# Kernel optimization log

Hardware: AMD Instinct MI355X
Metric: run time of the kernel (lower is better)

## Reference

```python
import jax, jax.numpy as jnp
import numpy as np

N, D, E, OUT = 10000, 15, 320, 30
H_INOUT = 5  # n_heads for in/out attention layers


def mha(q, k, v, wqkv, bqkv, wo, bo, nheads):
    # q,k,v: [B, L, E]; torch.nn.MultiheadAttention math (unbatched per node)
    B, L, Ed = q.shape
    hd = Ed // nheads
    wq, wk, wv = jnp.split(wqkv, 3, axis=0)
    bq, bk, bv = jnp.split(bqkv, 3)
    q2 = (q @ wq.T + bq).reshape(B, L, nheads, hd)
    k2 = (k @ wk.T + bk).reshape(B, -1, nheads, hd)
    v2 = (v @ wv.T + bv).reshape(B, -1, nheads, hd)
    scores = jnp.einsum('blhd,bmhd->bhlm', q2, k2) * (hd ** -0.5)
    a = jax.nn.softmax(scores, axis=-1)
    o = jnp.einsum('bhlm,bmhd->blhd', a, v2).reshape(B, L, Ed)
    return o @ wo.T + bo


def attn_layer(seq, Wq, Wk, Wv, wqkv, bqkv, wo, bo, nheads):
    # AttentionLayer: custom Q/K/V projections then MultiheadAttention
    return mha(seq @ Wq, seq @ Wk, seq @ Wv, wqkv, bqkv, wo, bo, nheads)


def setup_inputs() -> dict:
    key = jax.random.key(0)
    ks = jax.random.split(key, 24)
    s = 0.05  # scale params small for numerically stable softmax
    inp = {
        'X': jax.random.normal(ks[0], (N, E), jnp.float32),
        'in_idx': jax.random.randint(ks[1], (N, D), 0, N),
        'out_idx': jax.random.randint(ks[2], (N, D), 0, N),
        'in_Wq': jax.random.uniform(ks[3], (E, E)) * s,
        'in_Wk': jax.random.uniform(ks[4], (E, E)) * s,
        'in_Wv': jax.random.uniform(ks[5], (E, E)) * s,
        'in_qkv_w': jax.random.normal(ks[6], (3 * E, E)) * s,
        'in_qkv_b': jax.random.normal(ks[7], (3 * E,)) * s,
        'in_o_w': jax.random.normal(ks[8], (E, E)) * s,
        'in_o_b': jax.random.normal(ks[9], (E,)) * s,
        'out_Wq': jax.random.uniform(ks[10], (E, E)) * s,
        'out_Wk': jax.random.uniform(ks[11], (E, E)) * s,
        'out_Wv': jax.random.uniform(ks[12], (E, E)) * s,
        'out_qkv_w': jax.random.normal(ks[13], (3 * E, E)) * s,
        'out_qkv_b': jax.random.normal(ks[14], (3 * E,)) * s,
        'out_o_w': jax.random.normal(ks[15], (E, E)) * s,
        'out_o_b': jax.random.normal(ks[16], (E,)) * s,
        'fin_qkv_w': jax.random.normal(ks[17], (3 * E, E)) * s,
        'fin_qkv_b': jax.random.normal(ks[18], (3 * E,)) * s,
        'fin_o_w': jax.random.normal(ks[19], (E, E)) * s,
        'fin_o_b': jax.random.normal(ks[20], (E,)) * s,
        'W': jax.random.uniform(ks[21], (E, OUT)) * s,
    }
    return inp


def reference(X, in_idx, out_idx, in_Wq, in_Wk, in_Wv, in_qkv_w, in_qkv_b,
              in_o_w, in_o_b, out_Wq, out_Wk, out_Wv, out_qkv_w, out_qkv_b,
              out_o_w, out_o_b, fin_qkv_w, fin_qkv_b, fin_o_w, fin_o_b, W):
    # per-node sequence: [self ; neighbors] -> [N, D+1, E]
    seq_in = jnp.concatenate([X[:, None, :], X[in_idx]], axis=1)
    seq_out = jnp.concatenate([X[:, None, :], X[out_idx]], axis=1)
    a_in = attn_layer(seq_in, in_Wq, in_Wk, in_Wv, in_qkv_w, in_qkv_b,
                      in_o_w, in_o_b, H_INOUT)
    a_out = attn_layer(seq_out, out_Wq, out_Wk, out_Wv, out_qkv_w, out_qkv_b,
                       out_o_w, out_o_b, H_INOUT)
    att = jnp.concatenate([a_in, a_out], axis=1)  # [N, 2(D+1), E]
    fin = mha(att, att, att, fin_qkv_w, fin_qkv_b, fin_o_w, fin_o_b, 1)
    # first token of final attention per node -> project -> ELU
    return jax.nn.elu(fin[:, 0, :] @ W)
```

## Files before the change

kernel.cpp:

```cpp
#include <hip/hip_runtime.h>
#include <hip/hip_bf16.h>

typedef __hip_bfloat16 bf16;
typedef __bf16 nbf;
typedef nbf bf16x8 __attribute__((ext_vector_type(8)));
typedef float f32x4 __attribute__((ext_vector_type(4)));

#define NNODE 10000
#define DDEG  15
#define EE    320
#define LL    16
#define NH    5
#define HD    64
#define OUTD  30
#define PCOLS 1920
#define KF    642

__global__ void detect_dtype_kernel(const unsigned int* __restrict__ X, int* __restrict__ flag)
{
    __shared__ int cnt;
    if (threadIdx.x == 0) cnt = 0;
    __syncthreads();
    int local = 0;
    for (int i = threadIdx.x; i < 1024; i += 256) {
        unsigned int lo = X[i] & 0xFFFFu;
        int e = (int)((lo >> 7) & 0xFFu);
        if (e >= 100 && e <= 140) local++;
    }
    atomicAdd(&cnt, local);
    __syncthreads();
    if (threadIdx.x == 0) *flag = (cnt > 512) ? 1 : 0;
}

__global__ void convert_bf_kernel(const void* __restrict__ src, nbf* __restrict__ dst,
                                  int n, const int* __restrict__ flag)
{
    int i = blockIdx.x * 256 + threadIdx.x;
    if (i >= n) return;
    if (*flag) dst[i] = ((const nbf*)src)[i];
    else       dst[i] = (nbf)(((const float*)src)[i]);
}

#define NSEG 18
struct ConvTab {
    const void* src[NSEG];
    void*       dst[NSEG];
    int         n[NSEG];
    int         tobf[NSEG];
};

__global__ void convert_batch_kernel(ConvTab t, const int* __restrict__ flag)
{
    const int seg = blockIdx.y;
    const int i = blockIdx.x * 256 + threadIdx.x;
    if (i >= t.n[seg]) return;
    float v = (*flag) ? (float)(((const nbf*)t.src[seg])[i]) : ((const float*)t.src[seg])[i];
    if (t.tobf[seg]) ((nbf*)t.dst[seg])[i] = (nbf)v;
    else             ((float*)t.dst[seg])[i] = v;
}

__global__ __launch_bounds__(256) void transpose3_kernel(const void* s0, const void* s1,
        const void* s2, nbf* __restrict__ dstbase, const int* __restrict__ flag)
{
    const void* src = (blockIdx.z == 0) ? s0 : (blockIdx.z == 1) ? s1 : s2;
    nbf* dst = dstbase + (size_t)blockIdx.z * EE * EE;
    __shared__ nbf tile[32][33];
    const int bx = blockIdx.x * 32, by = blockIdx.y * 32;
    const int tx = threadIdx.x & 31, ty = threadIdx.x >> 5;
    const int f = *flag;
    #pragma unroll
    for (int i = 0; i < 4; ++i) {
        const int r = by + ty + i * 8;
        float v = f ? (float)(((const nbf*)src)[(long)r * EE + bx + tx])
                    : ((const float*)src)[(long)r * EE + bx + tx];
        tile[ty + i * 8][tx] = (nbf)v;
    }
    __syncthreads();
    #pragma unroll
    for (int i = 0; i < 4; ++i) {
        const int r = bx + ty + i * 8;
        dst[(long)r * EE + by + tx] = tile[tx][ty + i * 8];
    }
}

__device__ __forceinline__ void stor(float* p, float v) { *p = v; }
__device__ __forceinline__ void stor(bf16* p, float v) { *p = __float2bfloat16(v); }

template<bool AT, bool BT, typename OT>
__global__ __launch_bounds__(256) void gemm_k(const float* __restrict__ A, int lda,
                       const float* __restrict__ B, int ldb,
                       const float* __restrict__ bias,
                       OT* __restrict__ C, int ldc, int M, int Nn, int K)
{
    __shared__ float As[16][65];
    __shared__ float Bs[16][65];
    const int tid = threadIdx.x;
    const int tx = tid & 15, ty = tid >> 4;
    const int n0 = blockIdx.x * 64, m0 = blockIdx.y * 64;
    float acc[4][4] = {};
    for (int k0 = 0; k0 < K; k0 += 16) {
        if constexpr (AT) {
            for (int i = tid; i < 1024; i += 256) {
                int kk = i >> 6, r = i & 63;
                int gm = m0 + r, gk = k0 + kk;
                As[kk][r] = (gm < M && gk < K) ? A[(long)gk * lda + gm] : 0.f;
            }
        } else {
            for (int i = tid; i < 1024; i += 256) {
                int r = i >> 4, kk = i & 15;
                int gm = m0 + r, gk = k0 + kk;
                As[kk][r] = (gm < M && gk < K) ? A[(long)gm * lda + gk] : 0.f;
            }
        }
        if constexpr (BT) {
            for (int i = tid; i < 1024; i += 256) {
                int r = i >> 4, kk = i & 15;
                int gn = n0 + r, gk = k0 + kk;
                Bs[kk][r] = (gn < Nn && gk < K) ? B[(long)gn * ldb + gk] : 0.f;
            }
        } else {
            for (int i = tid; i < 1024; i += 256) {
                int kk = i >> 6, c = i & 63;
                int gk = k0 + kk, gn = n0 + c;
                Bs[kk][c] = (gk < K && gn < Nn) ? B[(long)gk * ldb + gn] : 0.f;
            }
        }
        __syncthreads();
        #pragma unroll
        for (int kk = 0; kk < 16; ++kk) {
            float ra[4], rb[4];
            #pragma unroll
            for (int a = 0; a < 4; ++a) ra[a] = As[kk][ty * 4 + a];
            #pragma unroll
            for (int b = 0; b < 4; ++b) rb[b] = Bs[kk][tx * 4 + b];
            #pragma unroll
            for (int a = 0; a < 4; ++a)
                #pragma unroll
                for (int b = 0; b < 4; ++b)
                    acc[a][b] += ra[a] * rb[b];
        }
        __syncthreads();
    }
    #pragma unroll
    for (int a = 0; a < 4; ++a) {
        int gm = m0 + ty * 4 + a;
        if (gm >= M) continue;
        #pragma unroll
        for (int b = 0; b < 4; ++b) {
            int gn = n0 + tx * 4 + b;
            if (gn >= Nn) continue;
            float v = acc[a][b] + (bias ? bias[gn] : 0.f);
            stor(&C[(long)gm * ldc + gn], v);
        }
    }
}

template<typename OT>
__global__ __launch_bounds__(256) void gemm_mfma(const nbf* __restrict__ A, int lda,
        const nbf* __restrict__ Bt, int ldb, const float* __restrict__ bias,
        OT* __restrict__ C, int ldc, int M, int Nn, int K)
{
    __shared__ __align__(16) nbf As[128][40];
    __shared__ __align__(16) nbf Bs[128][40];
    const int tid = threadIdx.x;
    const int lane = tid & 63, wave = tid >> 6;
    const int wr = (wave >> 1) * 64, wc = (wave & 1) * 64;
    const int m0 = blockIdx.y * 128, n0 = blockIdx.x * 128;
    const int lr = lane & 15, lq = lane >> 4;
    f32x4 acc[4][4];
    #pragma unroll
    for (int i = 0; i < 4; ++i)
        #pragma unroll
        for (int j = 0; j < 4; ++j) { acc[i][j][0]=0.f; acc[i][j][1]=0.f; acc[i][j][2]=0.f; acc[i][j][3]=0.f; }

    for (int k0 = 0; k0 < K; k0 += 32) {
        #pragma unroll
        for (int v = tid; v < 512; v += 256) {
            const int row = v >> 2, cv = (v & 3) << 3;
            const int gk = k0 + cv;
            {
                const int gm = m0 + row;
                bf16x8 val;
                if (gm < M && gk + 8 <= K) {
                    val = *(const bf16x8*)(A + (long)gm * lda + gk);
                } else {
                    union { bf16x8 v8; nbf e[8]; } u;
                    #pragma unroll
                    for (int j = 0; j < 8; ++j) {
                        float x = (gm < M && gk + j < K) ? (float)A[(long)gm * lda + gk + j] : 0.f;
                        u.e[j] = (nbf)x;
                    }
                    val = u.v8;
                }
                *(bf16x8*)&As[row][cv] = val;
            }
            {
                const int gn = n0 + row;
                bf16x8 val;
                if (gn < Nn && gk + 8 <= K) {
                    val = *(const bf16x8*)(Bt + (long)gn * ldb + gk);
                } else {
                    union { bf16x8 v8; nbf e[8]; } u;
                    #pragma unroll
                    for (int j = 0; j < 8; ++j) {
                        float x = (gn < Nn && gk + j < K) ? (float)Bt[(long)gn * ldb + gk + j] : 0.f;
                        u.e[j] = (nbf)x;
                    }
                    val = u.v8;
                }
                *(bf16x8*)&Bs[row][cv] = val;
            }
        }
        __syncthreads();
        bf16x8 af[4], bfv[4];
        #pragma unroll
        for (int i = 0; i < 4; ++i) af[i] = *(const bf16x8*)&As[wr + i * 16 + lr][lq * 8];
        #pragma unroll
        for (int j = 0; j < 4; ++j) bfv[j] = *(const bf16x8*)&Bs[wc + j * 16 + lr][lq * 8];
        #pragma unroll
        for (int i = 0; i < 4; ++i)
            #pragma unroll
            for (int j = 0; j < 4; ++j)
                acc[i][j] = __builtin_amdgcn_mfma_f32_16x16x32_bf16(af[i], bfv[j], acc[i][j], 0, 0, 0);
        __syncthreads();
    }
    #pragma unroll
    for (int i = 0; i < 4; ++i) {
        #pragma unroll
        for (int j = 0; j < 4; ++j) {
            const int gn = n0 + wc + j * 16 + lr;
            if (gn >= Nn) continue;
            const float bv = bias ? bias[gn] : 0.f;
            #pragma unroll
            for (int r = 0; r < 4; ++r) {
                const int gm = m0 + wr + i * 16 + lq * 4 + r;
                if (gm < M) stor(&C[(long)gm * ldc + gn], acc[i][j][r] + bv);
            }
        }
    }
}

#define NJOB 11
struct JobTab {
    const nbf* A[NJOB];
    const nbf* B[NJOB];
    nbf*       C[NJOB];
};

__global__ __launch_bounds__(256) void gemm_mfma_jobs(JobTab jt)
{
    const nbf* A  = jt.A[blockIdx.z];
    const nbf* Bt = jt.B[blockIdx.z];
    nbf* C        = jt.C[blockIdx.z];
    __shared__ __align__(16) nbf As[128][40];
    __shared__ __align__(16) nbf Bs[128][40];
    const int tid = threadIdx.x;
    const int lane = tid & 63, wave = tid >> 6;
    const int wr = (wave >> 1) * 64, wc = (wave & 1) * 64;
    const int m0 = blockIdx.y * 128, n0 = blockIdx.x * 128;
    const int lr = lane & 15, lq = lane >> 4;
    f32x4 acc[4][4];
    #pragma unroll
    for (int i = 0; i < 4; ++i)
        #pragma unroll
        for (int j = 0; j < 4; ++j) { acc[i][j][0]=0.f; acc[i][j][1]=0.f; acc[i][j][2]=0.f; acc[i][j][3]=0.f; }
    for (int k0 = 0; k0 < EE; k0 += 32) {
        #pragma unroll
        for (int v = tid; v < 512; v += 256) {
            const int row = v >> 2, cv = (v & 3) << 3;
            const int gk = k0 + cv;
            const int gm = m0 + row, gn = n0 + row;
            bf16x8 va = {}, vb = {};
            if (gm < EE) va = *(const bf16x8*)(A + (long)gm * EE + gk);
            if (gn < EE) vb = *(const bf16x8*)(Bt + (long)gn * EE + gk);
            *(bf16x8*)&As[row][cv] = va;
            *(bf16x8*)&Bs[row][cv] = vb;
        }
        __syncthreads();
        bf16x8 af[4], bfv[4];
        #pragma unroll
        for (int i = 0; i < 4; ++i) af[i] = *(const bf16x8*)&As[wr + i * 16 + lr][lq * 8];
        #pragma unroll
        for (int j = 0; j < 4; ++j) bfv[j] = *(const bf16x8*)&Bs[wc + j * 16 + lr][lq * 8];
        #pragma unroll
        for (int i = 0; i < 4; ++i)
            #pragma unroll
            for (int j = 0; j < 4; ++j)
                acc[i][j] = __builtin_amdgcn_mfma_f32_16x16x32_bf16(af[i], bfv[j], acc[i][j], 0, 0, 0);
        __syncthreads();
    }
    #pragma unroll
    for (int i = 0; i < 4; ++i)
        #pragma unroll
        for (int j = 0; j < 4; ++j) {
            const int gn = n0 + wc + j * 16 + lr;
            if (gn >= EE) continue;
            #pragma unroll
            for (int r = 0; r < 4; ++r) {
                const int gm = m0 + wr + i * 16 + lq * 4 + r;
                if (gm < EE) C[(long)gm * EE + gn] = (nbf)acc[i][j][r];
            }
        }
}

__global__ __launch_bounds__(320) void compose_bias_kernel(
        const float* __restrict__ in_o_b, const float* __restrict__ out_o_b,
        const float* __restrict__ fin_qkv_w, const float* __restrict__ fin_qkv_b,
        float* __restrict__ bqc_in, nbf* __restrict__ Kcat, nbf* __restrict__ VcatN)
{
    const int which = blockIdx.x;
    const int b = threadIdx.x;
    const float* ob = (which == 2 || which == 4) ? out_o_b : in_o_b;
    const int off = (which == 0) ? 0 : (which <= 2) ? 320 : 640;
    float acc = fin_qkv_b[off + b];
    const float* wr = fin_qkv_w + (long)(off + b) * EE;
    for (int e = 0; e < EE; ++e) acc += ob[e] * wr[e];
    if (which == 0)      bqc_in[b] = acc;
    else if (which == 1) Kcat[(long)640 * EE + b] = (nbf)acc;
    else if (which == 2) Kcat[(long)641 * EE + b] = (nbf)acc;
    else if (which == 3) VcatN[(long)640 * EE + b] = (nbf)acc;
    else                 VcatN[(long)641 * EE + b] = (nbf)acc;
}

__global__ void compose_bfin(const float* __restrict__ fin_o_b, const float* __restrict__ W,
                             float* __restrict__ bfin)
{
    int j = threadIdx.x;
    if (j >= OUTD) return;
    float acc = 0.f;
    for (int e = 0; e < EE; ++e) acc += fin_o_b[e] * W[e * OUTD + j];
    bfin[j] = acc;
}

__global__ void compose_bT(const float* __restrict__ bqc, const nbf* __restrict__ Kcat,
                           float* __restrict__ bT)
{
    int c = blockIdx.x * 256 + threadIdx.x;
    if (c >= KF) return;
    const nbf* kr = Kcat + (long)c * EE;
    float acc = 0.f;
    for (int b = 0; b < EE; ++b) acc += bqc[b] * (float)kr[b];
    bT[c] = acc;
}

__global__ void ut_prep_kernel(const float* __restrict__ WWT, nbf* __restrict__ Ut)
{
    int v = blockIdx.x * 256 + threadIdx.x;
    if (v >= 64 * EE) return;
    int n = v / EE, e = v % EE;
    float val = 0.f;
    if (n < OUTD) val = WWT[(long)n * KF + e];
    else if (n >= 32 && n < 32 + OUTD) val = WWT[(long)(n - 32) * KF + 320 + e];
    Ut[v] = (nbf)val;
}

__global__ __launch_bounds__(320) void attn1_kernel(const nbf* __restrict__ P,
                const int* __restrict__ in_idx, const int* __restrict__ out_idx,
                nbf* __restrict__ O, int node_base)
{
    const int bx = blockIdx.x;
    const int lnode = bx >> 1, dir = bx & 1;
    const int node = node_base + lnode;
    const int tid = threadIdx.x;
    const int lane = tid & 63, wave = tid >> 6;
    __shared__ __align__(16) nbf v_s[16][328];
    __shared__ __align__(16) nbf p_s[NH][16][16];
    const int* idx = dir ? out_idx : in_idx;
    const long coloff = (long)dir * 960;
    const int lr = lane & 15, lq = lane >> 4;
    #pragma unroll
    for (int v = tid; v < 640; v += 320) {
        const int row = v / 40, c8 = (v % 40) * 8;
        const int src = (row == 0) ? node : idx[node * DDEG + row - 1];
        *(bf16x8*)&v_s[row][c8] = *(const bf16x8*)(P + (long)src * PCOLS + coloff + 640 + c8);
    }
    const int msrc = (lr == 0) ? node : idx[node * DDEG + lr - 1];
    const nbf* prow = P + (long)msrc * PCOLS + coloff;
    f32x4 sc = {0.f, 0.f, 0.f, 0.f};
    #pragma unroll
    for (int c = 0; c < 2; ++c) {
        bf16x8 aq = *(const bf16x8*)(prow + wave * 64 + c * 32 + lq * 8);
        bf16x8 bk = *(const bf16x8*)(prow + 320 + wave * 64 + c * 32 + lq * 8);
        sc = __builtin_amdgcn_mfma_f32_16x16x32_bf16(aq, bk, sc, 0, 0, 0);
    }
    float pr[4], mx[4], sm[4];
    #pragma unroll
    for (int r = 0; r < 4; ++r) { pr[r] = sc[r] * 0.125f; mx[r] = pr[r]; }
    #pragma unroll
    for (int msk = 8; msk >= 1; msk >>= 1)
        #pragma unroll
        for (int r = 0; r < 4; ++r) mx[r] = fmaxf(mx[r], __shfl_xor(mx[r], msk));
    #pragma unroll
    for (int r = 0; r < 4; ++r) { pr[r] = __expf(pr[r] - mx[r]); sm[r] = pr[r]; }
    #pragma unroll
    for (int msk = 8; msk >= 1; msk >>= 1)
        #pragma unroll
        for (int r = 0; r < 4; ++r) sm[r] += __shfl_xor(sm[r], msk);
    #pragma unroll
    for (int r = 0; r < 4; ++r) p_s[wave][lq * 4 + r][lr] = (nbf)(pr[r] / sm[r]);
    union { bf16x8 v8; nbf e[8]; } pf;
    #pragma unroll
    for (int j = 0; j < 8; ++j) pf.e[j] = (nbf)0.f;
    if (lq < 2) pf.v8 = *(const bf16x8*)&p_s[wave][lr][lq * 8];
    __syncthreads();
    nbf* orow = O + (long)lnode * (32 * EE) + dir * (16 * EE);
    #pragma unroll
    for (int t = 0; t < 4; ++t) {
        const int e0 = wave * 64 + t * 16;
        union { bf16x8 v8; nbf e[8]; } af;
        #pragma unroll
        for (int j = 0; j < 8; ++j) af.e[j] = (nbf)0.f;
        if (lq < 2) {
            #pragma unroll
            for (int j = 0; j < 8; ++j) af.e[j] = v_s[lq * 8 + j][e0 + lr];
        }
        f32x4 ov = {0.f, 0.f, 0.f, 0.f};
        ov = __builtin_amdgcn_mfma_f32_16x16x32_bf16(af.v8, pf.v8, ov, 0, 0, 0);
        union { unsigned long long u; nbf e[4]; } o4;
        #pragma unroll
        for (int r = 0; r < 4; ++r) o4.e[r] = (nbf)ov[r];
        *(unsigned long long*)(orow + lr * EE + e0 + lq * 4) = o4.u;
    }
}

__global__ __launch_bounds__(256) void final_mega_kernel(const nbf* __restrict__ O,
        const float* __restrict__ T, const nbf* __restrict__ Ut,
        const float* __restrict__ WWT, const float* __restrict__ bfin,
        void* __restrict__ out, long obase, int ncnt, const int* __restrict__ flag)
{
    const int i0 = blockIdx.x * 4;
    const int tid = threadIdx.x;
    const int lane = tid & 63, wave = tid >> 6;
    const int node = i0 + wave;
    const int nodec = (node < ncnt) ? node : (ncnt - 1);
    __shared__ float t_s[4][KF];
    __shared__ float s_lds[4][32];
    for (int v = tid; v < 4 * KF; v += 256) {
        const int nn = v / KF;
        const int nc = (i0 + nn < ncnt) ? (i0 + nn) : (ncnt - 1);
        t_s[nn][v % KF] = T[(long)nc * KF + (v % KF)];
    }
    __syncthreads();
    const int lr = lane & 15, lq = lane >> 4;
    const nbf* obase_p = O + (long)nodec * (32 * EE);
    f32x4 acc[2][2];
    #pragma unroll
    for (int a = 0; a < 2; ++a)
        #pragma unroll
        for (int b = 0; b < 2; ++b) { acc[a][b][0]=0.f; acc[a][b][1]=0.f; acc[a][b][2]=0.f; acc[a][b][3]=0.f; }
    float s_part[2] = {0.f, 0.f};
    #pragma unroll
    for (int k0 = 0; k0 < EE; k0 += 32) {
        bf16x8 af[2], bfv[4];
        #pragma unroll
        for (int mt = 0; mt < 2; ++mt)
            af[mt] = *(const bf16x8*)(obase_p + (long)(mt * 16 + lr) * EE + k0 + lq * 8);
        #pragma unroll
        for (int nt = 0; nt < 4; ++nt)
            bfv[nt] = *(const bf16x8*)(Ut + (long)(nt * 16 + lr) * EE + k0 + lq * 8);
        #pragma unroll
        for (int mt = 0; mt < 2; ++mt)
            #pragma unroll
            for (int pp = 0; pp < 2; ++pp)
                acc[mt][pp] = __builtin_amdgcn_mfma_f32_16x16x32_bf16(af[mt], bfv[mt * 2 + pp], acc[mt][pp], 0, 0, 0);
        #pragma unroll
        for (int mt = 0; mt < 2; ++mt) {
            const float* tp = &t_s[wave][mt * 320 + k0 + lq * 8];
            #pragma unroll
            for (int j = 0; j < 8; ++j) s_part[mt] += (float)af[mt][j] * tp[j];
        }
    }
    #pragma unroll
    for (int mt = 0; mt < 2; ++mt) {
        s_part[mt] += __shfl_xor(s_part[mt], 16);
        s_part[mt] += __shfl_xor(s_part[mt], 32);
    }
    if (lq == 0) {
        s_lds[wave][lr]      = (s_part[0] + t_s[wave][640]) * 0.05590169943749474f;
        s_lds[wave][16 + lr] = (s_part[1] + t_s[wave][641]) * 0.05590169943749474f;
    }
    __syncthreads();
    float mx = -1e30f;
    #pragma unroll 4
    for (int m = 0; m < 32; ++m) mx = fmaxf(mx, s_lds[wave][m]);
    float esum = 0.f, a_in = 0.f, a_out = 0.f;
    #pragma unroll 4
    for (int m = 0; m < 32; ++m) {
        float e = __expf(s_lds[wave][m] - mx);
        esum += e;
        if (m < 16) a_in += e; else a_out += e;
    }
    const float inv = 1.f / esum;
    a_in *= inv; a_out *= inv;
    float pj[2] = {0.f, 0.f};
    #pragma unroll
    for (int r = 0; r < 4; ++r) {
        float A0 = __expf(s_lds[wave][lq * 4 + r] - mx) * inv;
        float A1 = __expf(s_lds[wave][16 + lq * 4 + r] - mx) * inv;
        pj[0] += A0 * acc[0][0][r] + A1 * acc[1][0][r];
        pj[1] += A0 * acc[0][1][r] + A1 * acc[1][1][r];
    }
    #pragma unroll
    for (int pp = 0; pp < 2; ++pp) {
        pj[pp] += __shfl_xor(pj[pp], 16);
        pj[pp] += __shfl_xor(pj[pp], 32);
    }
    if (lq == 0 && node < ncnt) {
        #pragma unroll
        for (int h = 0; h < 2; ++h) {
            const int j = h * 16 + lr;
            if (j < OUTD) {
                float r = pj[h] + a_in * WWT[(long)j * KF + 640]
                        + a_out * WWT[(long)j * KF + 641] + bfin[j];
                r = r > 0.f ? r : expm1f(r);
                if (*flag) ((bf16*)out)[obase + (long)node * OUTD + j] = __float2bfloat16(r);
                else       ((float*)out)[obase + (long)node * OUTD + j] = r;
            }
        }
    }
}

extern "C" void kernel_launch(void* const* d_in, const int* in_sizes, int n_in,
                              void* d_out, int out_size, void* d_ws, size_t ws_size,
                              hipStream_t stream)
{
    const int* in_idx  = (const int*)d_in[1];
    const int* out_idx = (const int*)d_in[2];

    char* p = (char*)d_ws;
    auto alloc = [&](size_t bytes) { char* r = p; p += (bytes + 255) & ~(size_t)255; return r; };
    const size_t EE2 = (size_t)EE * EE;
    int*   flag       = (int*)alloc(256);
    nbf*   X_bf       = (nbf*)alloc((size_t)NNODE * EE * 2);
    nbf*   qkvw6_bf   = (nbf*)alloc(6 * EE2 * 2);
    nbf*   Wg6_bf     = (nbf*)alloc(6 * EE2 * 2);
    nbf*   qkvw_fin_bf= (nbf*)alloc(3 * EE2 * 2);
    nbf*   owT        = (nbf*)alloc(3 * EE2 * 2);
    float* qkvw_fin_f = (float*)alloc(3 * EE2 * 4);
    float* qkvb_fin_f = (float*)alloc(3 * EE * 4);
    float* bcat       = (float*)alloc(PCOLS * 4);
    float* ob_in_f    = (float*)alloc(EE * 4);
    float* ob_out_f   = (float*)alloc(EE * 4);
    float* ob_fin_f   = (float*)alloc(EE * 4);
    float* W_f        = (float*)alloc((size_t)EE * OUTD * 4);
    float* ow_fin_f   = (float*)alloc(EE2 * 4);
    nbf*   AcatT  = (nbf*)alloc((size_t)PCOLS * EE * 2);
    nbf*   Qc_bf  = (nbf*)alloc(EE2 * 2);
    nbf*   Kcat   = (nbf*)alloc((size_t)KF * EE * 2);
    float* bqc_in = (float*)alloc(EE * 4);
    nbf*   M2T    = (nbf*)alloc((size_t)KF * EE * 2);
    float* bT     = (float*)alloc(KF * 4);
    nbf*   VcatN  = (nbf*)alloc((size_t)KF * EE * 2);
    nbf*   WfinT  = (nbf*)alloc((size_t)OUTD * EE * 2);
    float* WWT    = (float*)alloc((size_t)OUTD * KF * 4);
    float* bfin   = (float*)alloc(64 * 4);
    nbf*   Ut     = (nbf*)alloc((size_t)64 * EE * 2);
    nbf*   P      = (nbf*)alloc((size_t)NNODE * PCOLS * 2);
    size_t fixed = (size_t)(p - (char*)d_ws);

    const size_t per_node = (size_t)32 * EE * 2 + (size_t)KF * 4;
    size_t avail = (ws_size > fixed + 65536) ? (ws_size - fixed - 65536) : 0;
    long chunk_l = (long)(avail / (per_node + 8));
    chunk_l = (chunk_l / 4) * 4;
    int chunk = (chunk_l > NNODE) ? NNODE : (chunk_l < 4 ? 4 : (int)chunk_l);
    nbf*   O_c    = (nbf*)alloc((size_t)chunk * 32 * EE * 2);
    float* T_c    = (float*)alloc((size_t)chunk * KF * 4);

    dim3 blk(256);
    detect_dtype_kernel<<<1, blk, 0, stream>>>((const unsigned int*)d_in[0], flag);
    convert_bf_kernel<<<(NNODE * EE + 255) / 256, blk, 0, stream>>>(d_in[0], X_bf, NNODE * EE, flag);
    ConvTab ct;
    int s = 0;
    auto seg = [&](const void* src, void* dst, int n, int tobf) {
        ct.src[s] = src; ct.dst[s] = dst; ct.n[s] = n; ct.tobf[s] = tobf; ++s;
    };
    seg(d_in[6],  qkvw6_bf,           (int)(3 * EE2), 1);
    seg(d_in[13], qkvw6_bf + 3 * EE2, (int)(3 * EE2), 1);
    seg(d_in[3],  Wg6_bf + 0 * EE2, (int)EE2, 1);
    seg(d_in[4],  Wg6_bf + 1 * EE2, (int)EE2, 1);
    seg(d_in[5],  Wg6_bf + 2 * EE2, (int)EE2, 1);
    seg(d_in[10], Wg6_bf + 3 * EE2, (int)EE2, 1);
    seg(d_in[11], Wg6_bf + 4 * EE2, (int)EE2, 1);
    seg(d_in[12], Wg6_bf + 5 * EE2, (int)EE2, 1);
    seg(d_in[17], qkvw_fin_bf, (int)(3 * EE2), 1);
    seg(d_in[17], qkvw_fin_f,  (int)(3 * EE2), 0);
    seg(d_in[18], qkvb_fin_f, 3 * EE, 0);
    seg(d_in[7],  bcat,       3 * EE, 0);
    seg(d_in[14], bcat + 960, 3 * EE, 0);
    seg(d_in[9],  ob_in_f,  EE, 0);
    seg(d_in[16], ob_out_f, EE, 0);
    seg(d_in[20], ob_fin_f, EE, 0);
    seg(d_in[21], W_f, EE * OUTD, 0);
    seg(d_in[19], ow_fin_f, (int)EE2, 0);
    convert_batch_kernel<<<dim3((3 * (int)EE2 + 255) / 256, NSEG), blk, 0, stream>>>(ct, flag);
    transpose3_kernel<<<dim3(10, 10, 3), blk, 0, stream>>>(d_in[8], d_in[15], d_in[19], owT, flag);

    JobTab jt;
    for (int g = 0; g < 6; ++g) {
        jt.A[g] = qkvw6_bf + (size_t)g * EE2;
        jt.B[g] = Wg6_bf + (size_t)g * EE2;
        jt.C[g] = AcatT + (size_t)g * EE2;
    }
    jt.A[6] = owT;             jt.B[6] = qkvw_fin_bf;                      jt.C[6] = Qc_bf;
    jt.A[7] = owT;             jt.B[7] = qkvw_fin_bf + (size_t)320 * EE;   jt.C[7] = Kcat;
    jt.A[8] = owT + EE2;       jt.B[8] = qkvw_fin_bf + (size_t)320 * EE;   jt.C[8] = Kcat + (size_t)320 * EE;
    jt.A[9] = owT;             jt.B[9] = qkvw_fin_bf + (size_t)640 * EE;   jt.C[9] = VcatN;
    jt.A[10]= owT + EE2;       jt.B[10]= qkvw_fin_bf + (size_t)640 * EE;   jt.C[10]= VcatN + (size_t)320 * EE;
    gemm_mfma_jobs<<<dim3(3, 3, NJOB), blk, 0, stream>>>(jt);
    compose_bias_kernel<<<5, 320, 0, stream>>>(ob_in_f, ob_out_f, qkvw_fin_f, qkvb_fin_f,
                                               bqc_in, Kcat, VcatN);
    gemm_mfma<bf16><<<dim3(3, 6), blk, 0, stream>>>(
        Kcat, EE, Qc_bf, EE, nullptr, (bf16*)M2T, EE, KF, EE, EE);
    compose_bT<<<3, blk, 0, stream>>>(bqc_in, Kcat, bT);
    gemm_k<true, false, bf16><<<dim3(5, 1), blk, 0, stream>>>(
        W_f, OUTD, ow_fin_f, EE, nullptr, (bf16*)WfinT, EE, OUTD, EE, EE);
    gemm_mfma<float><<<dim3(6, 1), blk, 0, stream>>>(
        WfinT, EE, VcatN, EE, nullptr, WWT, KF, OUTD, KF, EE);
    compose_bfin<<<1, 64, 0, stream>>>(ob_fin_f, W_f, bfin);
    ut_prep_kernel<<<(64 * EE + 255) / 256, blk, 0, stream>>>(WWT, Ut);

    gemm_mfma<bf16><<<dim3(PCOLS / 128, (NNODE + 127) / 128), blk, 0, stream>>>(
        X_bf, EE, AcatT, EE, bcat, (bf16*)P, PCOLS, NNODE, PCOLS, EE);

    for (int base = 0; base < NNODE; base += chunk) {
        int cnt = (NNODE - base < chunk) ? (NNODE - base) : chunk;
        attn1_kernel<<<2 * cnt, dim3(320), 0, stream>>>(P, in_idx, out_idx, O_c, base);
        gemm_mfma<float><<<dim3((KF + 127) / 128, (cnt + 127) / 128), blk, 0, stream>>>(
            O_c, 32 * EE, M2T, EE, bT, T_c, KF, cnt, KF, EE);
        final_mega_kernel<<<(cnt + 3) / 4, blk, 0, stream>>>(
            O_c, T_c, Ut, WWT, bfin, d_out, (long)base * OUTD, cnt, flag);
    }
}
```

Baseline: 587.7 us.

## Fuse first-stage attention with final attention and avoid materializing O

Adds a small row0 kernel that computes only the first query token of the in-attention, which is all the final query projection needs. The T GEMM then runs on one row per node instead of the full 32-row O tensor. A single mega kernel per node recomputes both first-stage attentions, keeps the 32x320 outputs in shared memory, and runs the final softmax and output projection in place. This removes the large O round-trip through global memory and the chunked launch loop, at the cost of duplicating some first-stage attention work and using more shared memory per block.

```diff
diff --git a/kernel.cpp b/kernel.cpp
--- a/kernel.cpp
+++ b/kernel.cpp
@@ -15,6 +15,7 @@
 #define OUTD  30
 #define PCOLS 1920
 #define KF    642
+#define TST   644
 
 __global__ void detect_dtype_kernel(const unsigned int* __restrict__ X, int* __restrict__ flag)
 {
@@ -354,168 +355,187 @@
     Ut[v] = (nbf)val;
 }
 
-__global__ __launch_bounds__(320) void attn1_kernel(const nbf* __restrict__ P,
-                const int* __restrict__ in_idx, const int* __restrict__ out_idx,
-                nbf* __restrict__ O, int node_base)
-{
-    const int bx = blockIdx.x;
-    const int lnode = bx >> 1, dir = bx & 1;
-    const int node = node_base + lnode;
+__global__ __launch_bounds__(256) void row0_kernel(const nbf* __restrict__ P,
+        const int* __restrict__ in_idx, nbf* __restrict__ Orow0)
+{
+    const int tid = threadIdx.x, lane = tid & 63, wave = tid >> 6;
+    const int node = blockIdx.x * 4 + wave;
+    __shared__ float a_sh[4][16];
+    __shared__ int srcs_sh[4][16];
+    const int m = lane & 15, q4 = lane >> 4;
+    const int src = (m == 0) ? node : in_idx[node * DDEG + m - 1];
+    if (q4 == 0) srcs_sh[wave][m] = src;
+    const nbf* qrow = P + (long)node * PCOLS;
+    const nbf* krow = P + (long)src * PCOLS + 320;
+    #pragma unroll
+    for (int h = 0; h < NH; ++h) {
+        float s = 0.f;
+        bf16x8 q1 = *(const bf16x8*)(qrow + h * 64 + q4 * 16);
+        bf16x8 q2 = *(const bf16x8*)(qrow + h * 64 + q4 * 16 + 8);
+        bf16x8 k1 = *(const bf16x8*)(krow + h * 64 + q4 * 16);
+        bf16x8 k2 = *(const bf16x8*)(krow + h * 64 + q4 * 16 + 8);
+        #pragma unroll
+        for (int j = 0; j < 8; ++j)
+            s += (float)q1[j] * (float)k1[j] + (float)q2[j] * (float)k2[j];
+        s += __shfl_xor(s, 16);
+        s += __shfl_xor(s, 32);
+        s *= 0.125f;
+        float mxv = s;
+        #pragma unroll
+        for (int msk = 8; msk >= 1; msk >>= 1) mxv = fmaxf(mxv, __shfl_xor(mxv, msk));
+        float e = __expf(s - mxv);
+        float es = e;
+        #pragma unroll
+        for (int msk = 8; msk >= 1; msk >>= 1) es += __shfl_xor(es, msk);
+        if (q4 == 0) a_sh[wave][m] = e / es;
+        float o = 0.f;
+        #pragma unroll
+        for (int mm = 0; mm < 16; ++mm)
+            o += a_sh[wave][mm] * (float)P[(long)srcs_sh[wave][mm] * PCOLS + 640 + h * 64 + lane];
+        Orow0[(long)node * EE + h * 64 + lane] = (nbf)o;
+    }
+}
+
+__global__ __launch_bounds__(320) void mega_attn_kernel(const nbf* __restrict__ P,
+        const int* __restrict__ in_idx, const int* __restrict__ out_idx,
+        const float* __restrict__ T, const nbf* __restrict__ Ut,
+        const float* __restrict__ WWT, const float* __restrict__ bfin,
+        void* __restrict__ out, const int* __restrict__ flag)
+{
+    const int node = blockIdx.x;
     const int tid = threadIdx.x;
     const int lane = tid & 63, wave = tid >> 6;
+    __shared__ __align__(16) nbf o_s[32][328];
     __shared__ __align__(16) nbf v_s[16][328];
     __shared__ __align__(16) nbf p_s[NH][16][16];
-    const int* idx = dir ? out_idx : in_idx;
-    const long coloff = (long)dir * 960;
+    __shared__ float s_red[2][16][8];
+    __shared__ float s_fin[32];
+    __shared__ float a_s[32];
+    __shared__ float g_s[640];
     const int lr = lane & 15, lq = lane >> 4;
-    #pragma unroll
-    for (int v = tid; v < 640; v += 320) {
-        const int row = v / 40, c8 = (v % 40) * 8;
-        const int src = (row == 0) ? node : idx[node * DDEG + row - 1];
-        *(bf16x8*)&v_s[row][c8] = *(const bf16x8*)(P + (long)src * PCOLS + coloff + 640 + c8);
-    }
-    const int msrc = (lr == 0) ? node : idx[node * DDEG + lr - 1];
-    const nbf* prow = P + (long)msrc * PCOLS + coloff;
-    f32x4 sc = {0.f, 0.f, 0.f, 0.f};
-    #pragma unroll
-    for (int c = 0; c < 2; ++c) {
-        bf16x8 aq = *(const bf16x8*)(prow + wave * 64 + c * 32 + lq * 8);
-        bf16x8 bk = *(const bf16x8*)(prow + 320 + wave * 64 + c * 32 + lq * 8);
-        sc = __builtin_amdgcn_mfma_f32_16x16x32_bf16(aq, bk, sc, 0, 0, 0);
-    }
-    float pr[4], mx[4], sm[4];
-    #pragma unroll
-    for (int r = 0; r < 4; ++r) { pr[r] = sc[r] * 0.125f; mx[r] = pr[r]; }
-    #pragma unroll
-    for (int msk = 8; msk >= 1; msk >>= 1)
-        #pragma unroll
-        for (int r = 0; r < 4; ++r) mx[r] = fmaxf(mx[r], __shfl_xor(mx[r], msk));
-    #pragma unroll
-    for (int r = 0; r < 4; ++r) { pr[r] = __expf(pr[r] - mx[r]); sm[r] = pr[r]; }
-    #pragma unroll
-    for (int msk = 8; msk >= 1; msk >>= 1)
-        #pragma unroll
-        for (int r = 0; r < 4; ++r) sm[r] += __shfl_xor(sm[r], msk);
-    #pragma unroll
-    for (int r = 0; r < 4; ++r) p_s[wave][lq * 4 + r][lr] = (nbf)(pr[r] / sm[r]);
-    union { bf16x8 v8; nbf e[8]; } pf;
-    #pragma unroll
-    for (int j = 0; j < 8; ++j) pf.e[j] = (nbf)0.f;
-    if (lq < 2) pf.v8 = *(const bf16x8*)&p_s[wave][lr][lq * 8];
+    const float* Trow = T + (long)node * TST;
+
+    for (int d = 0; d < 2; ++d) {
+        if (d) __syncthreads();
+        const int* idx = d ? out_idx : in_idx;
+        const long coloff = (long)d * 960;
+        #pragma unroll
+        for (int v = tid; v < 640; v += 320) {
+            const int row = v / 40, c8 = (v % 40) * 8;
+            const int src = (row == 0) ? node : idx[node * DDEG + row - 1];
+            *(bf16x8*)&v_s[row][c8] = *(const bf16x8*)(P + (long)src * PCOLS + coloff + 640 + c8);
+        }
+        const int msrc = (lr == 0) ? node : idx[node * DDEG + lr - 1];
+        const nbf* prow = P + (long)msrc * PCOLS + coloff;
+        f32x4 sc = {0.f, 0.f, 0.f, 0.f};
+        #pragma unroll
+        for (int c = 0; c < 2; ++c) {
+            bf16x8 aq = *(const bf16x8*)(prow + wave * 64 + c * 32 + lq * 8);
+            bf16x8 bk = *(const bf16x8*)(prow + 320 + wave * 64 + c * 32 + lq * 8);
+            sc = __builtin_amdgcn_mfma_f32_16x16x32_bf16(aq, bk, sc, 0, 0, 0);
+        }
+        float pr[4], mx4[4], sm4[4];
+        #pragma unroll
+        for (int r = 0; r < 4; ++r) { pr[r] = sc[r] * 0.125f; mx4[r] = pr[r]; }
+        #pragma unroll
+        for (int msk = 8; msk >= 1; msk >>= 1)
+            #pragma unroll
+            for (int r = 0; r < 4; ++r) mx4[r] = fmaxf(mx4[r], __shfl_xor(mx4[r], msk));
+        #pragma unroll
+        for (int r = 0; r < 4; ++r) { pr[r] = __expf(pr[r] - mx4[r]); sm4[r] = pr[r]; }
+        #pragma unroll
+        for (int msk = 8; msk >= 1; msk >>= 1)
+            #pragma unroll
+            for (int r = 0; r < 4; ++r) sm4[r] += __shfl_xor(sm4[r], msk);
+        #pragma unroll
+        for (int r = 0; r < 4; ++r) p_s[wave][lq * 4 + r][lr] = (nbf)(pr[r] / sm4[r]);
+        union { bf16x8 v8; nbf e[8]; } pf;
+        #pragma unroll
+        for (int j = 0; j < 8; ++j) pf.e[j] = (nbf)0.f;
+        if (lq < 2) pf.v8 = *(const bf16x8*)&p_s[wave][lr][lq * 8];
+        __syncthreads();
+        float spart = 0.f;
+        #pragma unroll
+        for (int t = 0; t < 4; ++t) {
+            const int e0 = wave * 64 + t * 16;
+            union { bf16x8 v8; nbf e[8]; } af;
+            #pragma unroll
+            for (int j = 0; j < 8; ++j) af.e[j] = (nbf)0.f;
+            if (lq < 2) {
+                #pragma unroll
+                for (int j = 0; j < 8; ++j) af.e[j] = v_s[lq * 8 + j][e0 + lr];
+            }
+            f32x4 ov = {0.f, 0.f, 0.f, 0.f};
+            ov = __builtin_amdgcn_mfma_f32_16x16x32_bf16(af.v8, pf.v8, ov, 0, 0, 0);
+            union { unsigned long long u; nbf e[4]; } o4;
+            #pragma unroll
+            for (int r = 0; r < 4; ++r) o4.e[r] = (nbf)ov[r];
+            *(unsigned long long*)&o_s[d * 16 + lr][e0 + lq * 4] = o4.u;
+            f32x4 tv = *(const f32x4*)(Trow + d * 320 + e0 + lq * 4);
+            spart += ov[0] * tv[0] + ov[1] * tv[1] + ov[2] * tv[2] + ov[3] * tv[3];
+        }
+        spart += __shfl_xor(spart, 16);
+        spart += __shfl_xor(spart, 32);
+        if (lq == 0) s_red[d][lr][wave] = spart;
+    }
     __syncthreads();
-    nbf* orow = O + (long)lnode * (32 * EE) + dir * (16 * EE);
-    #pragma unroll
-    for (int t = 0; t < 4; ++t) {
-        const int e0 = wave * 64 + t * 16;
-        union { bf16x8 v8; nbf e[8]; } af;
-        #pragma unroll
-        for (int j = 0; j < 8; ++j) af.e[j] = (nbf)0.f;
-        if (lq < 2) {
-            #pragma unroll
-            for (int j = 0; j < 8; ++j) af.e[j] = v_s[lq * 8 + j][e0 + lr];
-        }
-        f32x4 ov = {0.f, 0.f, 0.f, 0.f};
-        ov = __builtin_amdgcn_mfma_f32_16x16x32_bf16(af.v8, pf.v8, ov, 0, 0, 0);
-        union { unsigned long long u; nbf e[4]; } o4;
-        #pragma unroll
-        for (int r = 0; r < 4; ++r) o4.e[r] = (nbf)ov[r];
-        *(unsigned long long*)(orow + lr * EE + e0 + lq * 4) = o4.u;
-    }
-}
-
-__global__ __launch_bounds__(256) void final_mega_kernel(const nbf* __restrict__ O,
-        const float* __restrict__ T, const nbf* __restrict__ Ut,
-        const float* __restrict__ WWT, const float* __restrict__ bfin,
-        void* __restrict__ out, long obase, int ncnt, const int* __restrict__ flag)
-{
-    const int i0 = blockIdx.x * 4;
-    const int tid = threadIdx.x;
-    const int lane = tid & 63, wave = tid >> 6;
-    const int node = i0 + wave;
-    const int nodec = (node < ncnt) ? node : (ncnt - 1);
-    __shared__ float t_s[4][KF];
-    __shared__ float s_lds[4][32];
-    for (int v = tid; v < 4 * KF; v += 256) {
-        const int nn = v / KF;
-        const int nc = (i0 + nn < ncnt) ? (i0 + nn) : (ncnt - 1);
-        t_s[nn][v % KF] = T[(long)nc * KF + (v % KF)];
-    }
-    __syncthreads();
-    const int lr = lane & 15, lq = lane >> 4;
-    const nbf* obase_p = O + (long)nodec * (32 * EE);
-    f32x4 acc[2][2];
-    #pragma unroll
-    for (int a = 0; a < 2; ++a)
-        #pragma unroll
-        for (int b = 0; b < 2; ++b) { acc[a][b][0]=0.f; acc[a][b][1]=0.f; acc[a][b][2]=0.f; acc[a][b][3]=0.f; }
-    float s_part[2] = {0.f, 0.f};
-    #pragma unroll
-    for (int k0 = 0; k0 < EE; k0 += 32) {
-        bf16x8 af[2], bfv[4];
-        #pragma unroll
-        for (int mt = 0; mt < 2; ++mt)
-            af[mt] = *(const bf16x8*)(obase_p + (long)(mt * 16 + lr) * EE + k0 + lq * 8);
-        #pragma unroll
-        for (int nt = 0; nt < 4; ++nt)
-            bfv[nt] = *(const bf16x8*)(Ut + (long)(nt * 16 + lr) * EE + k0 + lq * 8);
-        #pragma unroll
-        for (int mt = 0; mt < 2; ++mt)
-            #pragma unroll
-            for (int pp = 0; pp < 2; ++pp)
-                acc[mt][pp] = __builtin_amdgcn_mfma_f32_16x16x32_bf16(af[mt], bfv[mt * 2 + pp], acc[mt][pp], 0, 0, 0);
-        #pragma unroll
-        for (int mt = 0; mt < 2; ++mt) {
-            const float* tp = &t_s[wave][mt * 320 + k0 + lq * 8];
-            #pragma unroll
-            for (int j = 0; j < 8; ++j) s_part[mt] += (float)af[mt][j] * tp[j];
-        }
-    }
-    #pragma unroll
-    for (int mt = 0; mt < 2; ++mt) {
-        s_part[mt] += __shfl_xor(s_part[mt], 16);
-        s_part[mt] += __shfl_xor(s_part[mt], 32);
-    }
-    if (lq == 0) {
-        s_lds[wave][lr]      = (s_part[0] + t_s[wave][640]) * 0.05590169943749474f;
-        s_lds[wave][16 + lr] = (s_part[1] + t_s[wave][641]) * 0.05590169943749474f;
+    if (tid < 32) {
+        const int d = tid >> 4, m = tid & 15;
+        float s = 0.f;
+        #pragma unroll
+        for (int w = 0; w < NH; ++w) s += s_red[d][m][w];
+        s += Trow[640 + d];
+        s_fin[tid] = s * 0.05590169943749474f;
     }
     __syncthreads();
     float mx = -1e30f;
     #pragma unroll 4
-    for (int m = 0; m < 32; ++m) mx = fmaxf(mx, s_lds[wave][m]);
+    for (int m = 0; m < 32; ++m) mx = fmaxf(mx, s_fin[m]);
     float esum = 0.f, a_in = 0.f, a_out = 0.f;
     #pragma unroll 4
     for (int m = 0; m < 32; ++m) {
-        float e = __expf(s_lds[wave][m] - mx);
+        float e = __expf(s_fin[m] - mx);
         esum += e;
         if (m < 16) a_in += e; else a_out += e;
     }
     const float inv = 1.f / esum;
     a_in *= inv; a_out *= inv;
-    float pj[2] = {0.f, 0.f};
-    #pragma unroll
-    for (int r = 0; r < 4; ++r) {
-        float A0 = __expf(s_lds[wave][lq * 4 + r] - mx) * inv;
-        float A1 = __expf(s_lds[wave][16 + lq * 4 + r] - mx) * inv;
-        pj[0] += A0 * acc[0][0][r] + A1 * acc[1][0][r];
-        pj[1] += A0 * acc[0][1][r] + A1 * acc[1][1][r];
-    }
-    #pragma unroll
-    for (int pp = 0; pp < 2; ++pp) {
-        pj[pp] += __shfl_xor(pj[pp], 16);
-        pj[pp] += __shfl_xor(pj[pp], 32);
-    }
-    if (lq == 0 && node < ncnt) {
-        #pragma unroll
-        for (int h = 0; h < 2; ++h) {
-            const int j = h * 16 + lr;
-            if (j < OUTD) {
-                float r = pj[h] + a_in * WWT[(long)j * KF + 640]
-                        + a_out * WWT[(long)j * KF + 641] + bfin[j];
-                r = r > 0.f ? r : expm1f(r);
-                if (*flag) ((bf16*)out)[obase + (long)node * OUTD + j] = __float2bfloat16(r);
-                else       ((float*)out)[obase + (long)node * OUTD + j] = r;
-            }
+    if (tid < 32) a_s[tid] = __expf(s_fin[tid] - mx) * inv;
+    __syncthreads();
+    #pragma unroll
+    for (int v = tid; v < 640; v += 320) {
+        const int mbase = (v < 320) ? 0 : 16;
+        const int e = (v < 320) ? v : v - 320;
+        float g = 0.f;
+        #pragma unroll
+        for (int m2 = 0; m2 < 16; ++m2)
+            g += a_s[mbase + m2] * (float)o_s[mbase + m2][e];
+        g_s[v] = g;
+    }
+    __syncthreads();
+    const int j = tid >> 3, sub = tid & 7;
+    if (j < OUTD) {
+        const nbf* u_in  = Ut + (long)j * EE;
+        const nbf* u_out = Ut + (long)(32 + j) * EE;
+        float acc = 0.f;
+        for (int c = sub; c < 40; c += 8) {
+            bf16x8 uv = *(const bf16x8*)(u_in + c * 8);
+            bf16x8 uo = *(const bf16x8*)(u_out + c * 8);
+            #pragma unroll
+            for (int jj = 0; jj < 8; ++jj) {
+                acc += g_s[c * 8 + jj] * (float)uv[jj];
+                acc += g_s[320 + c * 8 + jj] * (float)uo[jj];
+            }
+        }
+        acc += __shfl_down(acc, 4, 8);
+        acc += __shfl_down(acc, 2, 8);
+        acc += __shfl_down(acc, 1, 8);
+        if (sub == 0) {
+            float r = acc + a_in * WWT[(long)j * KF + 640]
+                    + a_out * WWT[(long)j * KF + 641] + bfin[j];
+            r = r > 0.f ? r : expm1f(r);
+            if (*flag) ((bf16*)out)[(long)node * OUTD + j] = __float2bfloat16(r);
+            else       ((float*)out)[(long)node * OUTD + j] = r;
         }
     }
 }
@@ -556,15 +576,8 @@
     float* bfin   = (float*)alloc(64 * 4);
     nbf*   Ut     = (nbf*)alloc((size_t)64 * EE * 2);
     nbf*   P      = (nbf*)alloc((size_t)NNODE * PCOLS * 2);
-    size_t fixed = (size_t)(p - (char*)d_ws);
-
-    const size_t per_node = (size_t)32 * EE * 2 + (size_t)KF * 4;
-    size_t avail = (ws_size > fixed + 65536) ? (ws_size - fixed - 65536) : 0;
-    long chunk_l = (long)(avail / (per_node + 8));
-    chunk_l = (chunk_l / 4) * 4;
-    int chunk = (chunk_l > NNODE) ? NNODE : (chunk_l < 4 ? 4 : (int)chunk_l);
-    nbf*   O_c    = (nbf*)alloc((size_t)chunk * 32 * EE * 2);
-    float* T_c    = (float*)alloc((size_t)chunk * KF * 4);
+    nbf*   Orow0  = (nbf*)alloc((size_t)NNODE * EE * 2);
+    float* Tm     = (float*)alloc((size_t)NNODE * TST * 4);
 
     dim3 blk(256);
     detect_dtype_kernel<<<1, blk, 0, stream>>>((const unsigned int*)d_in[0], flag);
@@ -622,12 +635,11 @@
     gemm_mfma<bf16><<<dim3(PCOLS / 128, (NNODE + 127) / 128), blk, 0, stream>>>(
         X_bf, EE, AcatT, EE, bcat, (bf16*)P, PCOLS, NNODE, PCOLS, EE);
 
-    for (int base = 0; base < NNODE; base += chunk) {
-        int cnt = (NNODE - base < chunk) ? (NNODE - base) : chunk;
-        attn1_kernel<<<2 * cnt, dim3(320), 0, stream>>>(P, in_idx, out_idx, O_c, base);
-        gemm_mfma<float><<<dim3((KF + 127) / 128, (cnt + 127) / 128), blk, 0, stream>>>(
-            O_c, 32 * EE, M2T, EE, bT, T_c, KF, cnt, KF, EE);
-        final_mega_kernel<<<(cnt + 3) / 4, blk, 0, stream>>>(
-            O_c, T_c, Ut, WWT, bfin, d_out, (long)base * OUTD, cnt, flag);
-    }
-}
+    row0_kernel<<<NNODE / 4, blk, 0, stream>>>(P, in_idx, Orow0);
+
+    gemm_mfma<float><<<dim3((KF + 127) / 128, (NNODE + 127) / 128), blk, 0, stream>>>(
+        Orow0, EE, M2T, EE, bT, Tm, TST, NNODE, KF, EE);
+
+    mega_attn_kernel<<<NNODE, dim3(320), 0, stream>>>(
+        P, in_idx, out_idx, Tm, Ut, WWT, bfin, d_out, flag);
+}
```

Result: no change. 593.6 us (+1.0%).
